# Performance work log

Hardware: AMD Instinct MI355X
Metric: run time of the kernel (lower is better)

Reference implementation:

```python
import jax, jax.numpy as jnp
import numpy as np

EPS = 1e-8


def box2corners(box):
    # box: (B, N, 5) = (x, y, w, h, angle_rad) -> corners (B, N, 4, 2)
    x, y, w, h, a = (box[..., i] for i in range(5))
    xs = jnp.array([0.5, -0.5, -0.5, 0.5], box.dtype) * w[..., None]
    ys = jnp.array([0.5, 0.5, -0.5, -0.5], box.dtype) * h[..., None]
    cos, sin = jnp.cos(a)[..., None], jnp.sin(a)[..., None]
    cx = xs * cos - ys * sin + x[..., None]
    cy = xs * sin + ys * cos + y[..., None]
    return jnp.stack([cx, cy], axis=-1)


def edge_intersections(c1, c2):
    # all 4x4 edge-pair segment intersections -> pts (B,N,16,2), mask (B,N,16)
    p = c1[..., :, None, :]                                  # (B,N,4,1,2)
    r = (jnp.roll(c1, -1, axis=-2) - c1)[..., :, None, :]     # edge dirs of box1
    q = c2[..., None, :, :]                                  # (B,N,1,4,2)
    s = (jnp.roll(c2, -1, axis=-2) - c2)[..., None, :, :]     # edge dirs of box2
    qp = q - p
    rxs = r[..., 0] * s[..., 1] - r[..., 1] * s[..., 0]
    t = (qp[..., 0] * s[..., 1] - qp[..., 1] * s[..., 0]) / (rxs + EPS)
    u = (qp[..., 0] * r[..., 1] - qp[..., 1] * r[..., 0]) / (rxs + EPS)
    mask = (t > 0.) & (t < 1.) & (u > 0.) & (u < 1.)
    pts = (p + t[..., None] * r) * mask[..., None]
    B, N = c1.shape[0], c1.shape[1]
    return pts.reshape(B, N, 16, 2), mask.reshape(B, N, 16)


def box_in_box(corners1, corners2):
    # True where corners of box1 lie inside box2 -> (B,N,4)
    a = corners2[..., 0:1, :]
    b = corners2[..., 1:2, :]
    d = corners2[..., 3:4, :]
    ab, ad, am = b - a, d - a, corners1 - a
    p_ab = jnp.sum(ab * am, -1) / (jnp.sum(ab * ab, -1) + EPS)
    p_ad = jnp.sum(ad * am, -1) / (jnp.sum(ad * ad, -1) + EPS)
    tol = 1e-6
    return (p_ab > -tol) & (p_ab < 1. + tol) & (p_ad > -tol) & (p_ad < 1. + tol)


def convex_area(verts, mask):
    # shoelace area of valid vertices, sorted CCW by angle around their mean
    m = mask.astype(verts.dtype)
    nv = jnp.sum(m, axis=-1)                                          # (B,N)
    mean = jnp.sum(verts * m[..., None], axis=-2) / jnp.maximum(nv, 1.)[..., None]
    v = verts - mean[..., None, :]
    ang = jnp.where(mask, jnp.arctan2(v[..., 1], v[..., 0]), 1e9)      # invalid sort last
    order = jnp.argsort(ang, axis=-1)
    v_s = jnp.take_along_axis(v, order[..., None], axis=-2)
    m_s = jnp.take_along_axis(mask, order, axis=-1)
    v_s = jnp.where(m_s[..., None], v_s, v_s[..., 0:1, :])  # pad tail with first vertex -> zero cross terms
    v_n = jnp.roll(v_s, -1, axis=-2)
    cross = v_s[..., 0] * v_n[..., 1] - v_s[..., 1] * v_n[..., 0]
    area = 0.5 * jnp.abs(jnp.sum(cross, axis=-1))
    return jnp.where(nv >= 3., area, 0.)


def diff_iou_rotated_2d(box1, box2):
    c1, c2 = box2corners(box1), box2corners(box2)
    pts, m_int = edge_intersections(c1, c2)
    m1 = box_in_box(c1, c2)
    m2 = box_in_box(c2, c1)
    verts = jnp.concatenate([c1, c2, pts], axis=-2)    # (B,N,24,2)
    mask = jnp.concatenate([m1, m2, m_int], axis=-1)   # (B,N,24)
    inter = convex_area(verts, mask)
    area1 = box1[..., 2] * box1[..., 3]
    area2 = box2[..., 2] * box2[..., 3]
    union = area1 + area2 - inter
    return inter / (union + EPS)


def setup_inputs() -> dict:
    key = jax.random.key(0)
    k1, k2, k3 = jax.random.split(key, 3)
    B, A, W, H = 16, 3, 128, 128
    pred = jax.random.uniform(k1, (B, A, W, H, 5), dtype=jnp.float32)
    target = jax.random.uniform(k2, (B, A, W, H, 5), dtype=jnp.float32)
    pos_idx = jax.random.randint(k3, (B, A, W, H), 0, 2).astype(bool)
    return {"pred": pred, "target": target, "pos_idx": pos_idx}


def reference(pred, target, pos_idx):
    eps = 1e-7
    target = target.at[..., -1].set(jnp.deg2rad(target[..., -1] * 180. - 180.))
    pred = pred.at[..., -1].set(jnp.deg2rad(pred[..., -1]))
    bs, A, w, h = target.shape[:-1]
    ious = diff_iou_rotated_2d(pred.reshape(1, -1, 5), target.reshape(1, -1, 5))
    ious = jnp.clip(ious.reshape(bs, A, w, h), eps, 1. - eps)
    m = pos_idx.astype(ious.dtype)
    # mode == 'linear': loss = 1 - iou, mean over positive samples
    loss = jnp.sum((1. - ious) * m) / jnp.maximum(jnp.sum(m), 1.)
    return loss, ious
```

## Files before the change

### kernel.cpp

```cpp
#include <hip/hip_runtime.h>

#define FEPS 1e-8f
#define ELEMS 4
#define NSLOTS 32

__device__ __forceinline__ void clip_edge_accum(
    float px, float py, float dx, float dy,
    float cx, float cy, float ux, float uy,
    float hw, float hh, float& sum)
{
    float rx = px - cx, ry = py - cy;
    float a0 = rx * ux + ry * uy;
    float b0 = dx * ux + dy * uy;
    float a1 = -rx * uy + ry * ux;
    float b1 = -dx * uy + dy * ux;

    float t0 = 0.0f, t1 = 1.0f;
    bool reject = false;
    {
        bool par = fabsf(b0) < 1e-12f;
        float inv = 1.0f / (par ? 1.0f : b0);
        float tA = (hw - a0) * inv, tB = (-hw - a0) * inv;
        t0 = par ? t0 : fmaxf(t0, fminf(tA, tB));
        t1 = par ? t1 : fminf(t1, fmaxf(tA, tB));
        reject = reject || (par && (fabsf(a0) > hw));
    }
    {
        bool par = fabsf(b1) < 1e-12f;
        float inv = 1.0f / (par ? 1.0f : b1);
        float tA = (hh - a1) * inv, tB = (-hh - a1) * inv;
        t0 = par ? t0 : fmaxf(t0, fminf(tA, tB));
        t1 = par ? t1 : fminf(t1, fmaxf(tA, tB));
        reject = reject || (par && (fabsf(a1) > hh));
    }
    bool ok = (!reject) && (t1 > t0);
    float sx = px + t0 * dx, sy = py + t0 * dy;
    float ex = px + t1 * dx, ey = py + t1 * dy;
    sum += ok ? (sx * ey - ex * sy) : 0.0f;
}

__device__ __forceinline__ float one_iou(
    float p0, float p1, float p2, float p3, float p4,
    float t0, float t1, float t2, float t3, float t4)
{
    const float DEG = 0.017453292519943295f;
    float a1 = p4 * DEG;
    float a2 = (t4 * 180.0f - 180.0f) * DEG;
    float s1, c1_; sincosf(a1, &s1, &c1_);
    float s2, c2_; sincosf(a2, &s2, &c2_);

    float hw1 = 0.5f * p2, hh1 = 0.5f * p3;
    float hw2 = 0.5f * t2, hh2 = 0.5f * t3;

    const float SX[4] = {0.5f, -0.5f, -0.5f, 0.5f};
    const float SY[4] = {0.5f, 0.5f, -0.5f, -0.5f};
    float P1x[4], P1y[4], P2x[4], P2y[4];
    #pragma unroll
    for (int k = 0; k < 4; ++k) {
        float xs = SX[k] * p2, ys = SY[k] * p3;
        P1x[k] = xs * c1_ - ys * s1 + p0;
        P1y[k] = xs * s1 + ys * c1_ + p1;
        float xs2 = SX[k] * t2, ys2 = SY[k] * t3;
        P2x[k] = xs2 * c2_ - ys2 * s2 + t0;
        P2y[k] = xs2 * s2 + ys2 * c2_ + t1;
    }

    float sum = 0.0f;
    #pragma unroll
    for (int k = 0; k < 4; ++k) {
        int kn = (k + 1) & 3;
        clip_edge_accum(P1x[k], P1y[k], P1x[kn]-P1x[k], P1y[kn]-P1y[k],
                        t0, t1, c2_, s2, hw2, hh2, sum);
    }
    #pragma unroll
    for (int k = 0; k < 4; ++k) {
        int kn = (k + 1) & 3;
        clip_edge_accum(P2x[k], P2y[k], P2x[kn]-P2x[k], P2y[kn]-P2y[k],
                        p0, p1, c1_, s1, hw1, hh1, sum);
    }

    float inter = 0.5f * fabsf(sum);
    float uni = p2 * p3 + t2 * t3 - inter;
    float iou = inter / (uni + FEPS);
    return fminf(fmaxf(iou, 1e-7f), 1.0f - 1e-7f);
}

__global__ __launch_bounds__(256) void riou_kernel(
    const float* __restrict__ pred, const float* __restrict__ target,
    const int* __restrict__ pos_idx, float* __restrict__ out,
    char* __restrict__ ws, int n)
{
    int tid = blockIdx.x * blockDim.x + threadIdx.x;
    int base = tid * ELEMS;
    float lnum = 0.0f;
    int   lden = 0;

    if (base + ELEMS <= n) {
        union { float4 q[5]; float f[20]; } P, T;
        const float4* pp = (const float4*)(pred + (size_t)base * 5);
        const float4* tp = (const float4*)(target + (size_t)base * 5);
        #pragma unroll
        for (int k = 0; k < 5; ++k) { P.q[k] = pp[k]; T.q[k] = tp[k]; }
        union { int4 q; int i[4]; } M;
        M.q = *(const int4*)(pos_idx + base);

        #pragma unroll
        for (int e = 0; e < ELEMS; ++e) {
            float iou = one_iou(P.f[e*5+0], P.f[e*5+1], P.f[e*5+2],
                                P.f[e*5+3], P.f[e*5+4],
                                T.f[e*5+0], T.f[e*5+1], T.f[e*5+2],
                                T.f[e*5+3], T.f[e*5+4]);
            out[1 + base + e] = iou;
            int m = (M.i[e] != 0) ? 1 : 0;
            lnum += (1.0f - iou) * (float)m;
            lden += m;
        }
    } else {
        for (int e = 0; e < ELEMS; ++e) {
            int g = base + e;
            if (g < n) {
                float iou = one_iou(pred[g*5+0], pred[g*5+1], pred[g*5+2],
                                    pred[g*5+3], pred[g*5+4],
                                    target[g*5+0], target[g*5+1], target[g*5+2],
                                    target[g*5+3], target[g*5+4]);
                out[1 + g] = iou;
                int m = (pos_idx[g] != 0) ? 1 : 0;
                lnum += (1.0f - iou) * (float)m;
                lden += m;
            }
        }
    }

    #pragma unroll
    for (int off = 32; off > 0; off >>= 1) {
        lnum += __shfl_down(lnum, off);
        lden += __shfl_down(lden, off);
    }
    __shared__ float snum[4];
    __shared__ int   sden[4];
    int wave = threadIdx.x >> 6, lane = threadIdx.x & 63;
    if (lane == 0) { snum[wave] = lnum; sden[wave] = lden; }
    __syncthreads();
    if (threadIdx.x == 0) {
        float bn = snum[0] + snum[1] + snum[2] + snum[3];
        int   bd = sden[0] + sden[1] + sden[2] + sden[3];
        char* slot = ws + (size_t)(blockIdx.x & (NSLOTS - 1)) * 64;
        atomicAdd((double*)slot, (double)bn);
        atomicAdd((int*)(slot + 8), bd);
    }
}

__global__ void riou_finalize(const char* __restrict__ ws,
                              float* __restrict__ out)
{
    int lane = threadIdx.x;
    double num = 0.0; int den = 0;
    if (lane < NSLOTS) {
        const char* slot = ws + (size_t)lane * 64;
        num = *(const double*)slot;
        den = *(const int*)(slot + 8);
    }
    #pragma unroll
    for (int off = 32; off > 0; off >>= 1) {
        num += __shfl_down(num, off);
        den += __shfl_down(den, off);
    }
    if (lane == 0) out[0] = (float)(num / (double)max(den, 1));
}

extern "C" void kernel_launch(void* const* d_in, const int* in_sizes, int n_in,
                              void* d_out, int out_size, void* d_ws, size_t ws_size,
                              hipStream_t stream) {
    const float* pred   = (const float*)d_in[0];
    const float* target = (const float*)d_in[1];
    const int*   posidx = (const int*)d_in[2];
    float* out = (float*)d_out;

    int n = in_sizes[0] / 5;

    hipMemsetAsync(d_ws, 0, NSLOTS * 64, stream);

    int block = 256;
    int grid = (n + block * ELEMS - 1) / (block * ELEMS);
    riou_kernel<<<grid, block, 0, stream>>>(pred, target, posidx, out,
                                            (char*)d_ws, n);
    riou_finalize<<<1, 64, 0, stream>>>((const char*)d_ws, out);
}
```

Baseline: 94.25 us.

## Use one element per thread, fast sin/cos, and per-block partials reduction

Each thread now handles a single box pair with scalar loads instead of four pairs through float4 vector loads. The accurate sincosf calls are replaced with __sinf/__cosf intrinsics. The memset and the double atomics into 32 slots are replaced by per-block float2 partials, which a 256-thread finalize kernel reduces. This raises parallelism and removes the memset and atomic contention, at the cost of less vectorized loads, lower trig accuracy, and a larger final reduction.

```diff
diff --git a/kernel.cpp b/kernel.cpp
--- a/kernel.cpp
+++ b/kernel.cpp
@@ -1,8 +1,6 @@
 #include <hip/hip_runtime.h>
 
 #define FEPS 1e-8f
-#define ELEMS 4
-#define NSLOTS 32
 
 __device__ __forceinline__ void clip_edge_accum(
     float px, float py, float dx, float dy,
@@ -46,8 +44,8 @@
     const float DEG = 0.017453292519943295f;
     float a1 = p4 * DEG;
     float a2 = (t4 * 180.0f - 180.0f) * DEG;
-    float s1, c1_; sincosf(a1, &s1, &c1_);
-    float s2, c2_; sincosf(a2, &s2, &c2_);
+    float s1 = __sinf(a1), c1_ = __cosf(a1);
+    float s2 = __sinf(a2), c2_ = __cosf(a2);
 
     float hw1 = 0.5f * p2, hh1 = 0.5f * p3;
     float hw2 = 0.5f * t2, hh2 = 0.5f * t3;
@@ -88,47 +86,20 @@
 __global__ __launch_bounds__(256) void riou_kernel(
     const float* __restrict__ pred, const float* __restrict__ target,
     const int* __restrict__ pos_idx, float* __restrict__ out,
-    char* __restrict__ ws, int n)
+    float2* __restrict__ partials, int n)
 {
-    int tid = blockIdx.x * blockDim.x + threadIdx.x;
-    int base = tid * ELEMS;
-    float lnum = 0.0f;
-    int   lden = 0;
+    int gid = blockIdx.x * blockDim.x + threadIdx.x;
+    float lnum = 0.0f, lden = 0.0f;
 
-    if (base + ELEMS <= n) {
-        union { float4 q[5]; float f[20]; } P, T;
-        const float4* pp = (const float4*)(pred + (size_t)base * 5);
-        const float4* tp = (const float4*)(target + (size_t)base * 5);
-        #pragma unroll
-        for (int k = 0; k < 5; ++k) { P.q[k] = pp[k]; T.q[k] = tp[k]; }
-        union { int4 q; int i[4]; } M;
-        M.q = *(const int4*)(pos_idx + base);
-
-        #pragma unroll
-        for (int e = 0; e < ELEMS; ++e) {
-            float iou = one_iou(P.f[e*5+0], P.f[e*5+1], P.f[e*5+2],
-                                P.f[e*5+3], P.f[e*5+4],
-                                T.f[e*5+0], T.f[e*5+1], T.f[e*5+2],
-                                T.f[e*5+3], T.f[e*5+4]);
-            out[1 + base + e] = iou;
-            int m = (M.i[e] != 0) ? 1 : 0;
-            lnum += (1.0f - iou) * (float)m;
-            lden += m;
-        }
-    } else {
-        for (int e = 0; e < ELEMS; ++e) {
-            int g = base + e;
-            if (g < n) {
-                float iou = one_iou(pred[g*5+0], pred[g*5+1], pred[g*5+2],
-                                    pred[g*5+3], pred[g*5+4],
-                                    target[g*5+0], target[g*5+1], target[g*5+2],
-                                    target[g*5+3], target[g*5+4]);
-                out[1 + g] = iou;
-                int m = (pos_idx[g] != 0) ? 1 : 0;
-                lnum += (1.0f - iou) * (float)m;
-                lden += m;
-            }
-        }
+    if (gid < n) {
+        const float* p = pred + (size_t)gid * 5;
+        const float* t = target + (size_t)gid * 5;
+        float iou = one_iou(p[0], p[1], p[2], p[3], p[4],
+                            t[0], t[1], t[2], t[3], t[4]);
+        out[1 + gid] = iou;
+        float m = (pos_idx[gid] != 0) ? 1.0f : 0.0f;
+        lnum = (1.0f - iou) * m;
+        lden = m;
     }
 
     #pragma unroll
@@ -136,36 +107,40 @@
         lnum += __shfl_down(lnum, off);
         lden += __shfl_down(lden, off);
     }
-    __shared__ float snum[4];
-    __shared__ int   sden[4];
+    __shared__ float snum[4], sden[4];
     int wave = threadIdx.x >> 6, lane = threadIdx.x & 63;
     if (lane == 0) { snum[wave] = lnum; sden[wave] = lden; }
     __syncthreads();
     if (threadIdx.x == 0) {
         float bn = snum[0] + snum[1] + snum[2] + snum[3];
-        int   bd = sden[0] + sden[1] + sden[2] + sden[3];
-        char* slot = ws + (size_t)(blockIdx.x & (NSLOTS - 1)) * 64;
-        atomicAdd((double*)slot, (double)bn);
-        atomicAdd((int*)(slot + 8), bd);
+        float bd = sden[0] + sden[1] + sden[2] + sden[3];
+        partials[blockIdx.x] = make_float2(bn, bd);
     }
 }
 
-__global__ void riou_finalize(const char* __restrict__ ws,
-                              float* __restrict__ out)
+__global__ __launch_bounds__(256) void riou_finalize(
+    const float2* __restrict__ partials, int nb, float* __restrict__ out)
 {
-    int lane = threadIdx.x;
-    double num = 0.0; int den = 0;
-    if (lane < NSLOTS) {
-        const char* slot = ws + (size_t)lane * 64;
-        num = *(const double*)slot;
-        den = *(const int*)(slot + 8);
+    double num = 0.0, den = 0.0;
+    for (int i = threadIdx.x; i < nb; i += 256) {
+        float2 p = partials[i];
+        num += (double)p.x;
+        den += (double)p.y;
     }
     #pragma unroll
     for (int off = 32; off > 0; off >>= 1) {
         num += __shfl_down(num, off);
         den += __shfl_down(den, off);
     }
-    if (lane == 0) out[0] = (float)(num / (double)max(den, 1));
+    __shared__ double dn[4], dd[4];
+    int wave = threadIdx.x >> 6, lane = threadIdx.x & 63;
+    if (lane == 0) { dn[wave] = num; dd[wave] = den; }
+    __syncthreads();
+    if (threadIdx.x == 0) {
+        double n2 = dn[0] + dn[1] + dn[2] + dn[3];
+        double d2 = dd[0] + dd[1] + dd[2] + dd[3];
+        out[0] = (float)(n2 / fmax(d2, 1.0));
+    }
 }
 
 extern "C" void kernel_launch(void* const* d_in, const int* in_sizes, int n_in,
@@ -178,11 +153,11 @@
 
     int n = in_sizes[0] / 5;
 
-    hipMemsetAsync(d_ws, 0, NSLOTS * 64, stream);
+    int block = 256;
+    int grid = (n + block - 1) / block;
+    float2* partials = (float2*)d_ws;
 
-    int block = 256;
-    int grid = (n + block * ELEMS - 1) / (block * ELEMS);
     riou_kernel<<<grid, block, 0, stream>>>(pred, target, posidx, out,
-                                            (char*)d_ws, n);
-    riou_finalize<<<1, 64, 0, stream>>>((const char*)d_ws, out);
+                                            partials, n);
+    riou_finalize<<<1, block, 0, stream>>>(partials, grid, out);
 }
```

After: 94.16 us. No clear change (-0.1%).
